# Kernel tuning notes

Hardware: AMD Instinct MI355X
Metric: run time of the kernel (lower is better)

## Reference

```python
import jax, jax.numpy as jnp
import numpy as np

N_MODES = 64


def setup_inputs() -> dict:
    key = jax.random.key(0)
    ks = jax.random.split(key, 5)
    B, L, C, M = 32, 8192, 64, N_MODES
    scale = 1.0 / (C * M)
    return {
        "x": jax.random.normal(ks[0], (B, L, C), dtype=jnp.float32),
        "w_spec_real": jax.random.normal(ks[1], (C, C, M), dtype=jnp.float32) * scale,
        "w_spec_imag": jax.random.normal(ks[2], (C, C, M), dtype=jnp.float32) * scale,
        "pw_weight": jax.random.normal(ks[3], (C, C), dtype=jnp.float32) * (1.0 / np.sqrt(C)),
        "pw_bias": jax.random.normal(ks[4], (C,), dtype=jnp.float32) * 0.01,
    }


def reference(x, w_spec_real, w_spec_imag, pw_weight, pw_bias):
    # x: [B, L, C] -> [B, C, L] (matches torch transpose(1, 2))
    xt = jnp.swapaxes(x, 1, 2)
    L = xt.shape[-1]
    xf = jnp.fft.rfft(xt, axis=-1)            # [B, C, F] complex64, F = L//2 + 1
    F = xf.shape[-1]
    K = min(N_MODES, F)
    W = (w_spec_real + 1j * w_spec_imag).astype(xf.dtype)  # [Cin, Cout, M]
    # Batched replacement of the per-mode loop: [B,Cin,K] x [Cin,Cout,K] -> [B,Cout,K]
    tf_low = jnp.einsum('bik,iok->bok', xf[:, :, :K], W[:, :, :K])
    tf = jnp.zeros_like(xf).at[:, :, :K].set(tf_low)
    x_back = jnp.fft.irfft(tf, n=L, axis=-1)  # [B, C, L] real
    # pointwise conv (kernel_size=1): [Cout,Cin] x [B,Cin,L] + bias
    pw = jnp.einsum('oi,bil->bol', pw_weight, xt) + pw_bias[None, :, None]
    return jnp.swapaxes(x_back + pw, 1, 2)     # [B, L, C]
```

## Files before the change

### kernel.cpp

```cpp
#include <hip/hip_runtime.h>
#include <stdint.h>

#define L_     8192
#define NB     32
#define NC     64
#define SPLITK 16
#define CHUNK  (L_ / SPLITK)
#define SXPAD  520

#define BF_OFF  0
#define XF_OFF  (2u  << 20)
#define XR_OFF  (18u << 20)
#define WC_OFF  (19u << 20)

typedef __bf16 bf16x8 __attribute__((ext_vector_type(8)));
typedef float  f32x4  __attribute__((ext_vector_type(4)));

__device__ __forceinline__ unsigned short f2bf(float f) {
  union { float f; unsigned int i; } v; v.f = f;
  unsigned int r = v.i + 0x7fffu + ((v.i >> 16) & 1u);
  return (unsigned short)(r >> 16);
}
__device__ __forceinline__ f32x4 mfma16(bf16x8 a, bf16x8 b, f32x4 c) {
  return __builtin_amdgcn_mfma_f32_16x16x32_bf16(a, b, c, 0, 0, 0);
}

__global__ __launch_bounds__(256) void k0_bf(unsigned short* __restrict__ Bf,
                                             const uint2* __restrict__ wrsrc,
                                             uint2* __restrict__ wc) {
  const int t = blockIdx.x * 256 + threadIdx.x;
  const int e0 = t * 8;
  const int j = e0 >> 13, l0 = e0 & 8191, k = j >> 1;
  const float W0 = 6.283185307179586f / 8192.0f;
  const float a = (k == 0 ? 1.0f : 2.0f) * (1.0f / 8192.0f);
  uint32_t w[4];
  #pragma unroll
  for (int u = 0; u < 4; ++u) {
    float s0, c0, s1, c1;
    __sincosf((float)((k * (l0 + 2 * u)) & 8191) * W0, &s0, &c0);
    __sincosf((float)((k * (l0 + 2 * u + 1)) & 8191) * W0, &s1, &c1);
    const unsigned short b0 = f2bf((j & 1) ? (-a * s0) : (a * c0));
    const unsigned short b1 = f2bf((j & 1) ? (-a * s1) : (a * c1));
    w[u] = (uint32_t)b0 | ((uint32_t)b1 << 16);
  }
  uint4 v; v.x = w[0]; v.y = w[1]; v.z = w[2]; v.w = w[3];
  *(uint4*)(Bf + e0) = v;
  wc[t] = wrsrc[t];
}

__global__ __launch_bounds__(256) void k1_dft(const float* __restrict__ x,
                                              const unsigned short* __restrict__ Bf,
                                              float* __restrict__ XFP) {
  const int b = blockIdx.x >> 4;
  const int p = blockIdx.x & 15;
  const int l0 = p * CHUNK;
  const int t = threadIdx.x;
  const int wv = t >> 6, lane = t & 63, q = lane >> 4, n = lane & 15;
  __shared__ uint32_t sx[NC * SXPAD / 2];
  const float* xb = x + (size_t)b * L_ * NC;

  {
    const int g  = t & 15;
    const int r2 = t >> 4;
    #pragma unroll 4
    for (int s = 0; s < 16; ++s) {
      const int lrow = s * 32 + 2 * r2;
      const f32x4 u0 = *(const f32x4*)(xb + (size_t)(l0 + lrow) * NC + 4 * g);
      const f32x4 u1 = *(const f32x4*)(xb + (size_t)(l0 + lrow + 1) * NC + 4 * g);
      #pragma unroll
      for (int jj = 0; jj < 4; ++jj) {
        __bf16 pk2[2] = {(__bf16)u0[jj], (__bf16)u1[jj]};
        sx[(4 * g + jj) * (SXPAD / 2) + s * 16 + r2] = __builtin_bit_cast(uint32_t, pk2);
      }
    }
  }
  __syncthreads();

  f32x4 acc[2][4];
  #pragma unroll
  for (int i = 0; i < 2; ++i)
    #pragma unroll
    for (int jn = 0; jn < 4; ++jn) acc[i][jn] = (f32x4){0.f, 0.f, 0.f, 0.f};
  const unsigned short* sxu = (const unsigned short*)sx;

  const unsigned short* arow0 = Bf + (size_t)(wv * 32 + n) * L_ + l0 + q * 8;
  const unsigned short* arow1 = Bf + (size_t)(wv * 32 + 16 + n) * L_ + l0 + q * 8;

  bf16x8 afr0 = *(const bf16x8*)(arow0);
  bf16x8 afr1 = *(const bf16x8*)(arow1);

  for (int ks = 0; ks < CHUNK; ks += 32) {
    const int lb = ks + q * 8;
    bf16x8 bfr[4];
    #pragma unroll
    for (int nt = 0; nt < 4; ++nt)
      bfr[nt] = *(const bf16x8*)(sxu + (nt * 16 + n) * SXPAD + lb);
    const bf16x8 nafr0 = *(const bf16x8*)(arow0 + ks + 32);
    const bf16x8 nafr1 = *(const bf16x8*)(arow1 + ks + 32);
    #pragma unroll
    for (int nt = 0; nt < 4; ++nt)
      acc[0][nt] = mfma16(afr0, bfr[nt], acc[0][nt]);
    #pragma unroll
    for (int nt = 0; nt < 4; ++nt)
      acc[1][nt] = mfma16(afr1, bfr[nt], acc[1][nt]);
    afr0 = nafr0; afr1 = nafr1;
  }

  float* op = XFP + (size_t)(p * NB + b) * 8192;
  #pragma unroll
  for (int mt = 0; mt < 2; ++mt)
    #pragma unroll
    for (int nt = 0; nt < 4; ++nt)
      *(f32x4*)(op + (size_t)(nt * 16 + n) * 128 + (wv * 32 + mt * 16 + q * 4)) =
          acc[mt][nt];
}

__global__ __launch_bounds__(256) void k1b_red(const f32x4* __restrict__ XFP,
                                               f32x4* __restrict__ XFR) {
  const int idx = blockIdx.x * 256 + threadIdx.x;
  f32x4 s = XFP[idx];
  #pragma unroll
  for (int p = 1; p < SPLITK; ++p) {
    const f32x4 v = XFP[(size_t)p * 65536 + idx];
    s[0] += v[0]; s[1] += v[1]; s[2] += v[2]; s[3] += v[3];
  }
  XFR[idx] = s;
}

__global__ __launch_bounds__(256) void k2_mix(const float* __restrict__ XFR,
                                              const float* __restrict__ wc,
                                              const float* __restrict__ wi,
                                              const float* __restrict__ pww,
                                              uint32_t* __restrict__ tf_out) {
  const int b = blockIdx.x >> 3;
  const int og = blockIdx.x & 7;
  const int t = threadIdx.x;
  const int k = t & 63;
  const int wv = t >> 6;
  __shared__ float sxf[8192];
  {
    f32x4* d = (f32x4*)sxf;
    const f32x4* s = (const f32x4*)(XFR + (size_t)b * 8192);
    #pragma unroll
    for (int i = 0; i < 8; ++i) d[t + i * 256] = s[t + i * 256];
  }
  __syncthreads();
  #pragma unroll
  for (int oo = 0; oo < 2; ++oo) {
    const int o = og * 8 + wv * 2 + oo;
    float ar = 0.f, ai = 0.f;
    #pragma unroll 8
    for (int i = 0; i < 64; ++i) {
      const float2 xv  = *(const float2*)&sxf[i * 128 + 2 * k];
      const float  wrv = wc[(size_t)i * 4096 + o * 64 + k];
      const float  wiv = wi[(size_t)i * 4096 + o * 64 + k];
      ar = fmaf(xv.x, wrv, ar);  ar = fmaf(-xv.y, wiv, ar);
      ai = fmaf(xv.x, wiv, ai);  ai = fmaf(xv.y, wrv, ai);
    }
    uint32_t* row = tf_out + ((size_t)b * 64 + o) * 96;
    row[k] = (uint32_t)f2bf(ar) | ((uint32_t)f2bf(ai) << 16);
    if (k < 32)
      row[64 + k] = (uint32_t)f2bf(pww[o * 64 + 2 * k]) |
                    ((uint32_t)f2bf(pww[o * 64 + 2 * k + 1]) << 16);
  }
}

__global__ __launch_bounds__(256) void k3_out(const float* __restrict__ x,
                                              const unsigned short* __restrict__ tf,
                                              const float* __restrict__ bias,
                                              float* __restrict__ out) {
  const int b = blockIdx.x >> 6;
  const int lt = blockIdx.x & 63;
  const int t = threadIdx.x;
  const int wv = t >> 6;
  const int lane = t & 63;
  const int q = lane >> 4;
  const int n = lane & 15;
  const int l0 = lt * 128 + wv * 32;
  const float* xb = x + (size_t)b * L_ * NC;
  const unsigned short* tfb = tf + (size_t)b * 64 * 192;
  const float W0 = 6.283185307179586f / 8192.0f;
  const int lA = l0 + n;
  const int lB = l0 + 16 + n;

  const f32x4* pA0 = (const f32x4*)(xb + (size_t)lA * NC + q * 8);
  const f32x4* pB0 = (const f32x4*)(xb + (size_t)lB * NC + q * 8);
  const f32x4* pA1 = (const f32x4*)(xb + (size_t)lA * NC + 32 + q * 8);
  const f32x4* pB1 = (const f32x4*)(xb + (size_t)lB * NC + 32 + q * 8);
  const f32x4 xA00 = pA0[0], xA01 = pA0[1];
  const f32x4 xB00 = pB0[0], xB01 = pB0[1];
  const f32x4 xA10 = pA1[0], xA11 = pA1[1];
  const f32x4 xB10 = pB1[0], xB11 = pB1[1];

  __shared__ unsigned short stf[64 * 200];
  {
    uint4* dst = (uint4*)stf;
    const uint4* src = (const uint4*)tfb;
    #pragma unroll
    for (int i = 0; i < 6; ++i) {
      const int e4 = t + i * 256;
      const int row = e4 / 24, c4 = e4 - row * 24;
      dst[row * 25 + c4] = src[e4];
    }
  }
  __syncthreads();

  f32x4 acc[4][2];
  #pragma unroll
  for (int i = 0; i < 4; ++i)
    #pragma unroll
    for (int jn = 0; jn < 2; ++jn) acc[i][jn] = (f32x4){0.f, 0.f, 0.f, 0.f};

  #pragma unroll
  for (int s = 0; s < 6; ++s) {
    const int k0 = s * 32;
    bf16x8 b0, b1;
    if (s < 4) {
      #pragma unroll
      for (int jj = 0; jj < 4; ++jj) {
        const int kf = (k0 >> 1) + q * 4 + jj;
        float sv, cv;
        __sincosf((float)((kf * lA) & 8191) * W0, &sv, &cv);
        b0[2 * jj] = (__bf16)cv; b0[2 * jj + 1] = (__bf16)(-sv);
        __sincosf((float)((kf * lB) & 8191) * W0, &sv, &cv);
        b1[2 * jj] = (__bf16)cv; b1[2 * jj + 1] = (__bf16)(-sv);
      }
    } else if (s == 4) {
      #pragma unroll
      for (int jj = 0; jj < 4; ++jj) {
        b0[jj] = (__bf16)xA00[jj]; b0[4 + jj] = (__bf16)xA01[jj];
        b1[jj] = (__bf16)xB00[jj]; b1[4 + jj] = (__bf16)xB01[jj];
      }
    } else {
      #pragma unroll
      for (int jj = 0; jj < 4; ++jj) {
        b0[jj] = (__bf16)xA10[jj]; b0[4 + jj] = (__bf16)xA11[jj];
        b1[jj] = (__bf16)xB10[jj]; b1[4 + jj] = (__bf16)xB11[jj];
      }
    }
    #pragma unroll
    for (int mt = 0; mt < 4; ++mt) {
      const bf16x8 afr = *(const bf16x8*)(stf + (mt * 16 + n) * 200 + k0 + q * 8);
      acc[mt][0] = mfma16(afr, b0, acc[mt][0]);
      acc[mt][1] = mfma16(afr, b1, acc[mt][1]);
    }
  }
  float* ob = out + (size_t)b * L_ * NC;
  #pragma unroll
  for (int mt = 0; mt < 4; ++mt) {
    const f32x4 bv = *(const f32x4*)(bias + mt * 16 + q * 4);
    #pragma unroll
    for (int nt = 0; nt < 2; ++nt) {
      const int l = l0 + nt * 16 + n;
      f32x4 v = acc[mt][nt];
      v[0] += bv[0]; v[1] += bv[1]; v[2] += bv[2]; v[3] += bv[3];
      *(f32x4*)(ob + (size_t)l * NC + mt * 16 + q * 4) = v;
    }
  }
}

extern "C" void kernel_launch(void* const* d_in, const int* in_sizes, int n_in,
                              void* d_out, int out_size, void* d_ws, size_t ws_size,
                              hipStream_t stream) {
  (void)in_sizes; (void)n_in; (void)out_size; (void)d_ws; (void)ws_size;
  const float* x    = (const float*)d_in[0];
  float*       wr   = (float*)d_in[1];
  const float* wi   = (const float*)d_in[2];
  const float* pww  = (const float*)d_in[3];
  const float* bias = (const float*)d_in[4];
  float* out = (float*)d_out;

  char* ob = (char*)d_out;
  unsigned short* Bf  = (unsigned short*)(ob + BF_OFF);
  float*          XFP = (float*)(ob + XF_OFF);
  float*          XFR = (float*)(ob + XR_OFF);
  float*          WC  = (float*)(ob + WC_OFF);

  k0_bf   <<<512,         256, 0, stream>>>(Bf, (const uint2*)wr, (uint2*)WC);
  k1_dft  <<<NB * SPLITK, 256, 0, stream>>>(x, Bf, XFP);
  k1b_red <<<256,         256, 0, stream>>>((const f32x4*)XFP, (f32x4*)XFR);
  k2_mix  <<<NB * 8,      256, 0, stream>>>(XFR, WC, wi, pww, (uint32_t*)wr);
  k3_out  <<<NB * 64,     256, 0, stream>>>(x, (const unsigned short*)wr, bias, out);
}
```

Measured before the change: 163.1 us.

## Fuse split-K reduction into mixing kernel and remap DFT staging loads

Removes the separate split-K reduction kernel and its intermediate buffer; the mixing kernel now sums the 16 partial spectra directly while loading into shared memory. Each of the 8 output-group blocks per batch redundantly reduces the same partials, trading one launch and a write/read round trip for 8x redundant partial reads, which are likely cache-resident. Block indexing is reordered so blocks sharing a batch are spread apart, and the DFT kernel's x-load thread mapping is changed so consecutive lanes cover consecutive row pairs.

```diff
diff --git a/kernel.cpp b/kernel.cpp
--- a/kernel.cpp
+++ b/kernel.cpp
@@ -10,7 +10,6 @@
 
 #define BF_OFF  0
 #define XF_OFF  (2u  << 20)
-#define XR_OFF  (18u << 20)
 #define WC_OFF  (19u << 20)
 
 typedef __bf16 bf16x8 __attribute__((ext_vector_type(8)));
@@ -60,17 +59,17 @@
   const float* xb = x + (size_t)b * L_ * NC;
 
   {
-    const int g  = t & 15;
-    const int r2 = t >> 4;
+    const int c4 = t >> 4;
+    const int lp = t & 15;
     #pragma unroll 4
     for (int s = 0; s < 16; ++s) {
-      const int lrow = s * 32 + 2 * r2;
-      const f32x4 u0 = *(const f32x4*)(xb + (size_t)(l0 + lrow) * NC + 4 * g);
-      const f32x4 u1 = *(const f32x4*)(xb + (size_t)(l0 + lrow + 1) * NC + 4 * g);
+      const int lpair = s * 16 + lp;
+      const f32x4 u0 = *(const f32x4*)(xb + (size_t)(l0 + 2 * lpair) * NC + 4 * c4);
+      const f32x4 u1 = *(const f32x4*)(xb + (size_t)(l0 + 2 * lpair + 1) * NC + 4 * c4);
       #pragma unroll
       for (int jj = 0; jj < 4; ++jj) {
         __bf16 pk2[2] = {(__bf16)u0[jj], (__bf16)u1[jj]};
-        sx[(4 * g + jj) * (SXPAD / 2) + s * 16 + r2] = __builtin_bit_cast(uint32_t, pk2);
+        sx[(4 * c4 + jj) * (SXPAD / 2) + lpair] = __builtin_bit_cast(uint32_t, pk2);
       }
     }
   }
@@ -115,34 +114,31 @@
           acc[mt][nt];
 }
 
-__global__ __launch_bounds__(256) void k1b_red(const f32x4* __restrict__ XFP,
-                                               f32x4* __restrict__ XFR) {
-  const int idx = blockIdx.x * 256 + threadIdx.x;
-  f32x4 s = XFP[idx];
-  #pragma unroll
-  for (int p = 1; p < SPLITK; ++p) {
-    const f32x4 v = XFP[(size_t)p * 65536 + idx];
-    s[0] += v[0]; s[1] += v[1]; s[2] += v[2]; s[3] += v[3];
-  }
-  XFR[idx] = s;
-}
-
-__global__ __launch_bounds__(256) void k2_mix(const float* __restrict__ XFR,
-                                              const float* __restrict__ wc,
-                                              const float* __restrict__ wi,
-                                              const float* __restrict__ pww,
-                                              uint32_t* __restrict__ tf_out) {
-  const int b = blockIdx.x >> 3;
-  const int og = blockIdx.x & 7;
+__global__ __launch_bounds__(256) void k2f_mix(const float* __restrict__ XFP,
+                                               const float* __restrict__ wc,
+                                               const float* __restrict__ wi,
+                                               const float* __restrict__ pww,
+                                               uint32_t* __restrict__ tf_out) {
+  const int b  = blockIdx.x & 31;
+  const int og = blockIdx.x >> 5;
   const int t = threadIdx.x;
   const int k = t & 63;
   const int wv = t >> 6;
   __shared__ float sxf[8192];
   {
     f32x4* d = (f32x4*)sxf;
-    const f32x4* s = (const f32x4*)(XFR + (size_t)b * 8192);
-    #pragma unroll
-    for (int i = 0; i < 8; ++i) d[t + i * 256] = s[t + i * 256];
+    const f32x4* s0 = (const f32x4*)XFP + (size_t)b * 2048;
+    #pragma unroll
+    for (int i = 0; i < 8; ++i) {
+      const int idx = t + i * 256;
+      f32x4 s = s0[idx];
+      #pragma unroll
+      for (int p = 1; p < SPLITK; ++p) {
+        const f32x4 v = s0[(size_t)p * 65536 + idx];
+        s[0] += v[0]; s[1] += v[1]; s[2] += v[2]; s[3] += v[3];
+      }
+      d[idx] = s;
+    }
   }
   __syncthreads();
   #pragma unroll
@@ -273,12 +269,10 @@
   char* ob = (char*)d_out;
   unsigned short* Bf  = (unsigned short*)(ob + BF_OFF);
   float*          XFP = (float*)(ob + XF_OFF);
-  float*          XFR = (float*)(ob + XR_OFF);
   float*          WC  = (float*)(ob + WC_OFF);
 
   k0_bf   <<<512,         256, 0, stream>>>(Bf, (const uint2*)wr, (uint2*)WC);
   k1_dft  <<<NB * SPLITK, 256, 0, stream>>>(x, Bf, XFP);
-  k1b_red <<<256,         256, 0, stream>>>((const f32x4*)XFP, (f32x4*)XFR);
-  k2_mix  <<<NB * 8,      256, 0, stream>>>(XFR, WC, wi, pww, (uint32_t*)wr);
+  k2f_mix <<<NB * 8,      256, 0, stream>>>(XFP, WC, wi, pww, (uint32_t*)wr);
   k3_out  <<<NB * 64,     256, 0, stream>>>(x, (const unsigned short*)wr, bias, out);
 }
```

Result: slower. 167.0 us (+2.4%).
